# Kernel tuning notes

Hardware: AMD Instinct MI355X
Metric: run time of the kernel (lower is better)

## Reference

```python
import jax, jax.numpy as jnp
import numpy as np

EPS = 1e-7  # torchvision distance_box_iou_loss eps


def cxcywh_to_xyxy(b):
    cx, cy, w, h = b[..., 0], b[..., 1], b[..., 2], b[..., 3]
    return jnp.stack([cx - w / 2, cy - h / 2, cx + w / 2, cy + h / 2], axis=-1)


def iou_and_diou(b1, b2):
    # b1, b2: broadcastable [..., 4] in xyxy. Returns (plain iou, diou loss).
    x1, y1, x2, y2 = b1[..., 0], b1[..., 1], b1[..., 2], b1[..., 3]
    xg1, yg1, xg2, yg2 = b2[..., 0], b2[..., 1], b2[..., 2], b2[..., 3]
    xi1 = jnp.maximum(x1, xg1); yi1 = jnp.maximum(y1, yg1)
    xi2 = jnp.minimum(x2, xg2); yi2 = jnp.minimum(y2, yg2)
    inter = jnp.clip(xi2 - xi1, 0.0) * jnp.clip(yi2 - yi1, 0.0)
    union = (x2 - x1) * (y2 - y1) + (xg2 - xg1) * (yg2 - yg1) - inter
    iou = inter / union                 # ops.box_iou: no eps
    iou_e = inter / (union + EPS)       # distance_box_iou_loss: eps
    xc1 = jnp.minimum(x1, xg1); yc1 = jnp.minimum(y1, yg1)
    xc2 = jnp.maximum(x2, xg2); yc2 = jnp.maximum(y2, yg2)
    diag = (xc2 - xc1) ** 2 + (yc2 - yc1) ** 2 + EPS
    dist = ((x1 + x2 - xg1 - xg2) * 0.5) ** 2 + ((y1 + y2 - yg1 - yg2) * 0.5) ** 2
    return iou, 1.0 - iou_e + dist / diag


def bce(p, t):
    # torch binary_cross_entropy clamps log terms at -100
    lnp = jnp.maximum(jnp.log(p), -100.0)
    ln1 = jnp.maximum(jnp.log(1.0 - p), -100.0)
    return -(t * lnp + (1.0 - t) * ln1)


def hungarian(cost):
    # O(n^3) Hungarian (Kuhn-Munkres with potentials) on a square matrix.
    # Returns col assignment per row (row_ind = arange(n)). Matches scipy
    # linear_sum_assignment for square inputs.
    n = cost.shape[0]
    INF = np.inf
    u = np.zeros(n + 1); v = np.zeros(n + 1)
    p = np.zeros(n + 1, dtype=np.int64)
    way = np.zeros(n + 1, dtype=np.int64)
    for i in range(1, n + 1):
        p[0] = i
        j0 = 0
        minv = np.full(n + 1, INF)
        used = np.zeros(n + 1, dtype=bool)
        while True:
            used[j0] = True
            i0 = p[j0]
            cur = cost[i0 - 1] - u[i0] - v[1:]
            free = ~used[1:]
            upd = free & (cur < minv[1:])
            minv[1:] = np.where(upd, cur, minv[1:])
            way[1:] = np.where(upd, j0, way[1:])
            masked = np.where(free, minv[1:], INF)
            j1 = int(np.argmin(masked)) + 1
            delta = masked[j1 - 1]
            uidx = np.nonzero(used)[0]
            u[p[uidx]] += delta
            v[uidx] -= delta
            minv[1:] = np.where(free, minv[1:] - delta, minv[1:])
            j0 = j1
            if p[j0] == 0:
                break
        while j0:
            j1 = way[j0]
            p[j0] = p[j1]
            j0 = j1
    col_of_row = np.empty(n, dtype=np.int64)
    col_of_row[p[1:] - 1] = np.arange(n)
    return col_of_row


def build_cost_and_match(p, bbox_pred, labels_target, bbox_target):
    # Fused, fully vectorized replacement of the original O(N*M) python loop.
    pb = cxcywh_to_xyxy(bbox_pred)   # [B,N,4]
    tb = cxcywh_to_xyxy(bbox_target)  # [B,M,4]
    _, diou_pair = iou_and_diou(pb[:, :, None, :], tb[:, None, :, :])  # [B,N,M]
    # original uses reduction='mean' BCE/L1 over the batch -> batch-constant [N,M]
    label_cost = bce(p[:, :, None], labels_target[:, None, :]).mean(axis=0)  # [N,M]
    l1_cost = jnp.abs(bbox_pred[:, :, None, :] - bbox_target[:, None, :, :]).mean(axis=(0, 3))
    cost = diou_pair + label_cost[None] + l1_cost[None]  # [B,N,M]
    cost_np = np.asarray(jax.device_get(cost), dtype=np.float64)
    cols = np.stack([hungarian(cost_np[b]) for b in range(cost_np.shape[0])])
    return jnp.asarray(cols)  # [B,N]


def matched_losses(labels_pred, bbox_pred, labels_target, bbox_target, cols):
    p = jax.nn.sigmoid(labels_pred[..., 0])  # [B,N]
    B = p.shape[0]
    bi = jnp.arange(B)[:, None]
    # square matching: row indices are arange(N), only targets get permuted
    t_m = labels_target[bi, cols]   # [B,N]
    bt_m = bbox_target[bi, cols]    # [B,N,4]
    w = jax.lax.stop_gradient((t_m == 1.0).astype(p.dtype))  # positives mask
    iou_e, diou_e = iou_and_diou(cxcywh_to_xyxy(bbox_pred), cxcywh_to_xyxy(bt_m))
    wsum = w.sum()
    diou_loss = (diou_e * w).sum() / wsum
    iou = (iou_e * w).sum() / wsum
    label_loss = bce(p, t_m).mean()
    bbox_loss = (jnp.abs(bbox_pred - bt_m) * w[..., None]).sum() / (wsum * 4.0)
    return diou_loss + label_loss + bbox_loss, iou


def setup_inputs() -> dict:
    key = jax.random.key(0)
    k1, k2, k3, k4 = jax.random.split(key, 4)
    B, N, M = 64, 256, 256
    labels_pred = jax.random.normal(k1, (B, N, 1), dtype=jnp.float32)
    # cxcywh boxes in (0.05, 0.95) so areas/unions are strictly positive
    bbox_pred = jax.random.uniform(k2, (B, N, 4), dtype=jnp.float32) * 0.9 + 0.05
    labels_target = jax.random.randint(k3, (B, M), 0, 2).astype(jnp.float32)
    bbox_target = jax.random.uniform(k4, (B, M, 4), dtype=jnp.float32) * 0.9 + 0.05
    return {"labels_pred": labels_pred, "bbox_pred": bbox_pred,
            "labels_target": labels_target, "bbox_target": bbox_target}


def reference(labels_pred, bbox_pred, labels_target, bbox_target):
    p = jax.nn.sigmoid(labels_pred[..., 0])
    cols = build_cost_and_match(p, bbox_pred, labels_target, bbox_target)
    total_loss, iou = matched_losses(labels_pred, bbox_pred, labels_target, bbox_target, cols)
    return total_loss, iou
```

## Files before the change

### kernel.cpp

```cpp
#include <hip/hip_runtime.h>
#include <math.h>

#define BB 64
#define NN 256
#define MM 256
#define EPSF 1e-7f
#define ROWS_LDS 156


__device__ __forceinline__ void iou_diou(const float4 pb, const float4 tb,
                                         float& iou, float& diou) {
    float x1 = pb.x - pb.z * 0.5f, y1 = pb.y - pb.w * 0.5f;
    float x2 = pb.x + pb.z * 0.5f, y2 = pb.y + pb.w * 0.5f;
    float xg1 = tb.x - tb.z * 0.5f, yg1 = tb.y - tb.w * 0.5f;
    float xg2 = tb.x + tb.z * 0.5f, yg2 = tb.y + tb.w * 0.5f;
    float xi1 = fmaxf(x1, xg1), yi1 = fmaxf(y1, yg1);
    float xi2 = fminf(x2, xg2), yi2 = fminf(y2, yg2);
    float inter = fmaxf(xi2 - xi1, 0.f) * fmaxf(yi2 - yi1, 0.f);
    float uni = (x2 - x1) * (y2 - y1) + (xg2 - xg1) * (yg2 - yg1) - inter;
    iou = inter / uni;
    float iou_e = inter / (uni + EPSF);
    float xc1 = fminf(x1, xg1), yc1 = fminf(y1, yg1);
    float xc2 = fmaxf(x2, xg2), yc2 = fmaxf(y2, yg2);
    float dx = xc2 - xc1, dy = yc2 - yc1;
    float diag = dx * dx + dy * dy + EPSF;
    float ex = (x1 + x2 - xg1 - xg2) * 0.5f;
    float ey = (y1 + y2 - yg1 - yg2) * 0.5f;
    float dist = ex * ex + ey * ey;
    diou = 1.f - iou_e + dist / diag;
}

__device__ __forceinline__ unsigned long long dkey(double d, int j) {
    unsigned long long b = (unsigned long long)__double_as_longlong(d);
    b ^= (b >> 63) ? 0xFFFFFFFFFFFFFFFFULL : 0x8000000000000000ULL;
    return (b & ~511ULL) | (unsigned long long)j;
}
__device__ __forceinline__ double unkey(unsigned long long k) {
    unsigned long long b = k & ~511ULL;
    b ^= (b & 0x8000000000000000ULL) ? 0x8000000000000000ULL : 0xFFFFFFFFFFFFFFFFULL;
    return __longlong_as_double((long long)b);
}

#define SEL4I(s, a0, a1, a2, a3) ((s) == 0 ? (a0) : (s) == 1 ? (a1) : (s) == 2 ? (a2) : (a3))
#define SEL4D(s, a0, a1, a2, a3) ((s) == 0 ? (a0) : (s) == 1 ? (a1) : (s) == 2 ? (a2) : (a3))

__device__ __forceinline__ double readlane_d(double v, int lane) {
    unsigned long long b = (unsigned long long)__double_as_longlong(v);
    int lo = __builtin_amdgcn_readlane((int)(unsigned int)b, lane);
    int hi = __builtin_amdgcn_readlane((int)(unsigned int)(b >> 32), lane);
    return __longlong_as_double((long long)(((unsigned long long)(unsigned int)hi << 32) |
                                            (unsigned long long)(unsigned int)lo));
}

#define RED_DPP_K(CTRL)                                                                     \
    do {                                                                                    \
        int lo_ = (int)(unsigned int)ka, hi_ = (int)(unsigned int)(ka >> 32);               \
        int nlo_ = __builtin_amdgcn_update_dpp(lo_, lo_, CTRL, 0xF, 0xF, false);            \
        int nhi_ = __builtin_amdgcn_update_dpp(hi_, hi_, CTRL, 0xF, 0xF, false);            \
        unsigned long long ok_ = ((unsigned long long)(unsigned int)nhi_ << 32) |           \
                                 (unsigned long long)(unsigned int)nlo_;                    \
        if (ok_ < ka) ka = ok_;                                                             \
    } while (0)

#define RED_ALL()                                                                           \
    do {                                                                                    \
        RED_DPP_K(0x111); RED_DPP_K(0x112); RED_DPP_K(0x114); RED_DPP_K(0x118);             \
        RED_DPP_K(0x142); RED_DPP_K(0x143);                                                 \
        unsigned int klo_ = (unsigned int)__builtin_amdgcn_readlane((int)(unsigned int)ka, 63); \
        unsigned int khi_ = (unsigned int)__builtin_amdgcn_readlane((int)(unsigned int)(ka >> 32), 63); \
        ka = ((unsigned long long)khi_ << 32) | klo_;                                       \
    } while (0)

#define RED_U32_STEP(CTRL)                                                                  \
    do {                                                                                    \
        unsigned int n_ = (unsigned int)__builtin_amdgcn_update_dpp((int)kb, (int)kb, CTRL, 0xF, 0xF, false); \
        if (n_ < kb) kb = n_;                                                               \
    } while (0)
#define RED_U32_ALL()                                                                       \
    do {                                                                                    \
        RED_U32_STEP(0x111); RED_U32_STEP(0x112); RED_U32_STEP(0x114); RED_U32_STEP(0x118); \
        RED_U32_STEP(0x142); RED_U32_STEP(0x143);                                           \
        kb = (unsigned int)__builtin_amdgcn_readlane((int)kb, 63);                          \
    } while (0)

__global__ __launch_bounds__(256) void k_prep(const float* __restrict__ lp,
                                              float* __restrict__ A,
                                              float* __restrict__ C) {
    int idx = blockIdx.x * 256 + threadIdx.x;
    float x = lp[idx];
    float p = 1.f / (1.f + expf(-x));
    A[idx] = -fmaxf(logf(p), -100.f);
    C[idx] = -fmaxf(logf(1.f - p), -100.f);
}

__global__ __launch_bounds__(256) void k_nm(const float* __restrict__ A,
                                            const float* __restrict__ C,
                                            const float* __restrict__ bp,
                                            const float* __restrict__ bt,
                                            const float* __restrict__ lt,
                                            float* __restrict__ lc,
                                            float* __restrict__ l1c) {
    int n = blockIdx.x, m = threadIdx.x;
    float sl = 0.f, s1 = 0.f;
    for (int b = 0; b < BB; ++b) {
        float a = A[b * NN + n];
        float c = C[b * NN + n];
        float t = lt[b * MM + m];
        sl += t * a + (1.f - t) * c;
        float4 P = *reinterpret_cast<const float4*>(bp + ((size_t)b * NN + n) * 4);
        float4 T = *reinterpret_cast<const float4*>(bt + ((size_t)b * MM + m) * 4);
        s1 += fabsf(P.x - T.x) + fabsf(P.y - T.y) + fabsf(P.z - T.z) + fabsf(P.w - T.w);
    }
    lc[n * MM + m]  = sl * (1.f / 64.f);
    l1c[n * MM + m] = s1 * (1.f / 256.f);
}

__global__ __launch_bounds__(256) void k_cost(const float* __restrict__ bp,
                                              const float* __restrict__ bt,
                                              const float* __restrict__ lc,
                                              const float* __restrict__ l1c,
                                              float* __restrict__ cost) {
    int bn = blockIdx.x;
    int b = bn >> 8, n = bn & 255;
    int m = threadIdx.x;
    float4 P = *reinterpret_cast<const float4*>(bp + ((size_t)bn) * 4);
    float4 T = *reinterpret_cast<const float4*>(bt + ((size_t)b * MM + m) * 4);
    float iou, diou;
    iou_diou(P, T, iou, diou);
    cost[((size_t)bn << 8) + m] = diou + lc[(n << 8) + m] + l1c[(n << 8) + m];
}

__global__ __launch_bounds__(64) void k_hungarian(const float* __restrict__ cost,
                                                  int* __restrict__ cols) {
    const int b = blockIdx.x;
    const int lane = threadIdx.x;
    const float* Cm = cost + (size_t)b * NN * MM;
    const unsigned long long MAXK = 0xFFFFFFFFFFFFFFFFULL;
    const double INFD = __builtin_inf();

    __shared__ float ldsC[ROWS_LDS * MM];
    __shared__ float ldsU[NN];
    __shared__ int jofrow[NN + 1];
    __shared__ int matches[NN + 1];
    for (int r = lane; r <= NN; r += 64) { jofrow[r] = 0x7fffffff; matches[r] = 0; }
    __syncthreads();

    double cm0 = INFD, cm1 = INFD, cm2 = INFD, cm3 = INFD;
    int rm0 = 0, rm1 = 0, rm2 = 0, rm3 = 0;
    for (int i = 0; i < NN; ++i) {
        float4 cr = *reinterpret_cast<const float4*>(Cm + (size_t)i * MM + 4 * lane);
        if (i < ROWS_LDS) *reinterpret_cast<float4*>(&ldsC[i * MM + 4 * lane]) = cr;
        float rl = fminf(fminf(cr.x, cr.y), fminf(cr.z, cr.w));
        unsigned int kb = __float_as_uint(rl);
        RED_U32_ALL();
        float u0i = __uint_as_float(kb);
        if (lane == 0) ldsU[i] = u0i;
        double du = (double)u0i;
        double h0 = (double)cr.x - du;
        double h1 = (double)cr.y - du;
        double h2 = (double)cr.z - du;
        double h3 = (double)cr.w - du;
        if (h0 < cm0) { cm0 = h0; rm0 = i; }
        if (h1 < cm1) { cm1 = h1; rm1 = i; }
        if (h2 < cm2) { cm2 = h2; rm2 = i; }
        if (h3 < cm3) { cm3 = h3; rm3 = i; }
    }
    atomicMin(&jofrow[rm0 + 1], 4 * lane + 1);
    atomicMin(&jofrow[rm1 + 1], 4 * lane + 2);
    atomicMin(&jofrow[rm2 + 1], 4 * lane + 3);
    atomicMin(&jofrow[rm3 + 1], 4 * lane + 4);
    atomicAdd(&matches[rm0 + 1], 1);
    atomicAdd(&matches[rm1 + 1], 1);
    atomicAdd(&matches[rm2 + 1], 1);
    atomicAdd(&matches[rm3 + 1], 1);
    __syncthreads();

    double vj0 = cm0, vj1 = cm1, vj2 = cm2, vj3 = cm3;
    int pj0_ = (jofrow[rm0 + 1] == 4 * lane + 1) ? rm0 + 1 : 0;
    int pj1_ = (jofrow[rm1 + 1] == 4 * lane + 2) ? rm1 + 1 : 0;
    int pj2_ = (jofrow[rm2 + 1] == 4 * lane + 3) ? rm2 + 1 : 0;
    int pj3_ = (jofrow[rm3 + 1] == 4 * lane + 4) ? rm3 + 1 : 0;
    double up0 = pj0_ ? (double)ldsU[pj0_ - 1] : 0.0;
    double up1 = pj1_ ? (double)ldsU[pj1_ - 1] : 0.0;
    double up2 = pj2_ ? (double)ldsU[pj2_ - 1] : 0.0;
    double up3 = pj3_ ? (double)ldsU[pj3_ - 1] : 0.0;
    int wy0 = 0, wy1 = 0, wy2 = 0, wy3 = 0;

    unsigned long long am0 = __ballot(jofrow[1 + lane]       != 0x7fffffff);
    unsigned long long am1 = __ballot(jofrow[1 + 64 + lane]  != 0x7fffffff);
    unsigned long long am2 = __ballot(jofrow[1 + 128 + lane] != 0x7fffffff);
    unsigned long long am3 = __ballot(jofrow[1 + 192 + lane] != 0x7fffffff);

    for (int i = 1; i <= NN; ++i) {
        if (matches[i] != 1) continue;
        int j1 = jofrow[i];
        int o = (j1 - 1) >> 2, s = (j1 - 1) & 3;
        float4 cr;
        if (i - 1 < ROWS_LDS)
            cr = *reinterpret_cast<const float4*>(&ldsC[(i - 1) * MM + 4 * lane]);
        else
            cr = *reinterpret_cast<const float4*>(Cm + (size_t)(i - 1) * MM + 4 * lane);
        double du = (double)ldsU[i - 1];
        double h0 = ((double)cr.x - du) - vj0;
        double h1 = ((double)cr.y - du) - vj1;
        double h2 = ((double)cr.z - du) - vj2;
        double h3 = ((double)cr.w - du) - vj3;
        if (lane == o) {
            if (s == 0) h0 = INFD; else if (s == 1) h1 = INFD;
            else if (s == 2) h2 = INFD; else h3 = INFD;
        }
        double hm = fmin(fmin(h0, h1), fmin(h2, h3));
        unsigned long long ka = (unsigned long long)__double_as_longlong(hm);
        RED_ALL();
        double m = __longlong_as_double((long long)ka);
        if (lane == o) {
            if (s == 0)      { vj0 -= m; up0 += m; }
            else if (s == 1) { vj1 -= m; up1 += m; }
            else if (s == 2) { vj2 -= m; up2 += m; }
            else             { vj3 -= m; up3 += m; }
        }
    }

    for (int i = 1; i <= NN; ++i) {
        unsigned long long amv = (i <= 64) ? am0 : (i <= 128) ? am1 : (i <= 192) ? am2 : am3;
        if ((amv >> ((i - 1) & 63)) & 1ULL) continue;
        float4 cr;
        if (i - 1 < ROWS_LDS)
            cr = *reinterpret_cast<const float4*>(&ldsC[(i - 1) * MM + 4 * lane]);
        else
            cr = *reinterpret_cast<const float4*>(Cm + (size_t)(i - 1) * MM + 4 * lane);
        double du = (double)ldsU[i - 1];
        double h0 = ((double)cr.x - du) - vj0;
        double h1 = ((double)cr.y - du) - vj1;
        double h2 = ((double)cr.z - du) - vj2;
        double h3 = ((double)cr.w - du) - vj3;
        unsigned long long k0 = dkey(h0, 4 * lane + 1);
        unsigned long long k1 = dkey(h1, 4 * lane + 2);
        unsigned long long k2 = dkey(h2, 4 * lane + 3);
        unsigned long long k3 = dkey(h3, 4 * lane + 4);
        unsigned long long ea = k1 < k0 ? k1 : k0;
        unsigned long long eb = k3 < k2 ? k3 : k2;
        unsigned long long ka = eb < ea ? eb : ea;
        RED_ALL();
        int j1 = (int)(ka & 511ULL);
        int o1 = (j1 - 1) >> 2, s1 = (j1 - 1) & 3;
        int pcur = __builtin_amdgcn_readlane(SEL4I(s1, pj0_, pj1_, pj2_, pj3_), o1);
        if (pcur == 0) {
            double u_i = du + unkey(ka);
            if (lane == o1) {
                if (s1 == 0)      { pj0_ = i; up0 = u_i; }
                else if (s1 == 1) { pj1_ = i; up1 = u_i; }
                else if (s1 == 2) { pj2_ = i; up2 = u_i; }
                else              { pj3_ = i; up3 = u_i; }
            }
            unsigned long long bit = 1ULL << ((i - 1) & 63);
            if (i <= 64) am0 |= bit; else if (i <= 128) am1 |= bit;
            else if (i <= 192) am2 |= bit; else am3 |= bit;
        }
    }

    for (int i = 1; i <= NN; ++i) {
        unsigned long long amv = (i <= 64) ? am0 : (i <= 128) ? am1 : (i <= 192) ? am2 : am3;
        if ((amv >> ((i - 1) & 63)) & 1ULL) continue;

        double u_i = (double)ldsU[i - 1];
        double mv0 = INFD, mv1 = INFD, mv2 = INFD, mv3 = INFD;
        int used4 = 0;
        int j0 = 0;
        int i0 = i;
        double ui0 = u_i;

        for (int it = 0; it <= NN; ++it) {
            double uv0 = ui0 + vj0, uv1 = ui0 + vj1, uv2 = ui0 + vj2, uv3 = ui0 + vj3;
            float4 cr;
            if (i0 - 1 < ROWS_LDS)
                cr = *reinterpret_cast<const float4*>(&ldsC[(i0 - 1) * MM + 4 * lane]);
            else
                cr = *reinterpret_cast<const float4*>(Cm + (size_t)(i0 - 1) * MM + 4 * lane);

            if (!(used4 & 1)) { double cur = (double)cr.x - uv0; if (cur < mv0) { mv0 = cur; wy0 = j0; } }
            if (!(used4 & 2)) { double cur = (double)cr.y - uv1; if (cur < mv1) { mv1 = cur; wy1 = j0; } }
            if (!(used4 & 4)) { double cur = (double)cr.z - uv2; if (cur < mv2) { mv2 = cur; wy2 = j0; } }
            if (!(used4 & 8)) { double cur = (double)cr.w - uv3; if (cur < mv3) { mv3 = cur; wy3 = j0; } }

            unsigned long long k0 = (used4 & 1) ? MAXK : dkey(mv0, 4 * lane + 1);
            unsigned long long k1 = (used4 & 2) ? MAXK : dkey(mv1, 4 * lane + 2);
            unsigned long long k2 = (used4 & 4) ? MAXK : dkey(mv2, 4 * lane + 3);
            unsigned long long k3 = (used4 & 8) ? MAXK : dkey(mv3, 4 * lane + 4);

            unsigned long long ea = k1 < k0 ? k1 : k0;
            unsigned long long eb = k3 < k2 ? k3 : k2;
            unsigned long long ka = eb < ea ? eb : ea;

            RED_ALL();

            double delta = unkey(ka);
            int j1 = (int)(ka & 511ULL);
            int o1 = (j1 - 1) >> 2, s1 = (j1 - 1) & 3;
            int pa = __builtin_amdgcn_readlane(SEL4I(s1, pj0_, pj1_, pj2_, pj3_), o1);
            double ua = readlane_d(SEL4D(s1, up0, up1, up2, up3), o1);

            u_i += delta;
            if (used4 & 1) { up0 += delta; vj0 -= delta; } else { mv0 -= delta; }
            if (used4 & 2) { up1 += delta; vj1 -= delta; } else { mv1 -= delta; }
            if (used4 & 4) { up2 += delta; vj2 -= delta; } else { mv2 -= delta; }
            if (used4 & 8) { up3 += delta; vj3 -= delta; } else { mv3 -= delta; }

            j0 = j1;
            if (pa == 0) break;
            int ci = j1 - 1;
            if ((ci >> 2) == lane) used4 |= 1 << (ci & 3);
            i0 = pa;
            ui0 = ua;
        }

        int jj = j0;
        while (jj) {
            int o = (jj - 1) >> 2, s = (jj - 1) & 3;
            int wv = SEL4I(s, wy0, wy1, wy2, wy3);
            int jn = __builtin_amdgcn_readlane(wv, o);
            int pn; double un;
            if (jn == 0) { pn = i; un = u_i; }
            else {
                int o2 = (jn - 1) >> 2, s2 = (jn - 1) & 3;
                int pv = SEL4I(s2, pj0_, pj1_, pj2_, pj3_);
                double uv = SEL4D(s2, up0, up1, up2, up3);
                pn = __builtin_amdgcn_readlane(pv, o2);
                un = readlane_d(uv, o2);
            }
            if (lane == o) {
                if (s == 0)      { pj0_ = pn; up0 = un; }
                else if (s == 1) { pj1_ = pn; up1 = un; }
                else if (s == 2) { pj2_ = pn; up2 = un; }
                else             { pj3_ = pn; up3 = un; }
            }
            jj = jn;
        }
    }

    cols[b * NN + (pj0_ - 1)] = 4 * lane + 0;
    cols[b * NN + (pj1_ - 1)] = 4 * lane + 1;
    cols[b * NN + (pj2_ - 1)] = 4 * lane + 2;
    cols[b * NN + (pj3_ - 1)] = 4 * lane + 3;
}

__global__ __launch_bounds__(256) void k_loss(const float* __restrict__ lp,
                                              const float* __restrict__ bp,
                                              const float* __restrict__ lt,
                                              const float* __restrict__ bt,
                                              const int* __restrict__ cols,
                                              float* __restrict__ partials) {
    int b = blockIdx.x, n = threadIdx.x;
    int col = cols[b * NN + n];
    float x = lp[b * NN + n];
    float pp = 1.f / (1.f + expf(-x));
    float t = lt[b * MM + col];
    float4 P = *reinterpret_cast<const float4*>(bp + ((size_t)b * NN + n) * 4);
    float4 T = *reinterpret_cast<const float4*>(bt + ((size_t)b * MM + col) * 4);
    float w = (t == 1.f) ? 1.f : 0.f;
    float iou, diou;
    iou_diou(P, T, iou, diou);
    float bce = -(t * fmaxf(logf(pp), -100.f) + (1.f - t) * fmaxf(logf(1.f - pp), -100.f));
    float l1 = fabsf(P.x - T.x) + fabsf(P.y - T.y) + fabsf(P.z - T.z) + fabsf(P.w - T.w);

    float v0 = w, v1 = diou * w, v2 = iou * w, v3 = bce, v4 = l1 * w;
    #pragma unroll
    for (int mm = 1; mm < 64; mm <<= 1) {
        v0 += __shfl_xor(v0, mm); v1 += __shfl_xor(v1, mm);
        v2 += __shfl_xor(v2, mm); v3 += __shfl_xor(v3, mm);
        v4 += __shfl_xor(v4, mm);
    }
    __shared__ float red[4][5];
    int wid = n >> 6, lane = n & 63;
    if (lane == 0) { red[wid][0] = v0; red[wid][1] = v1; red[wid][2] = v2; red[wid][3] = v3; red[wid][4] = v4; }
    __syncthreads();
    if (n == 0) {
        float s0 = red[0][0] + red[1][0] + red[2][0] + red[3][0];
        float s1 = red[0][1] + red[1][1] + red[2][1] + red[3][1];
        float s2 = red[0][2] + red[1][2] + red[2][2] + red[3][2];
        float s3 = red[0][3] + red[1][3] + red[2][3] + red[3][3];
        float s4 = red[0][4] + red[1][4] + red[2][4] + red[3][4];
        partials[b * 8 + 0] = s0; partials[b * 8 + 1] = s1; partials[b * 8 + 2] = s2;
        partials[b * 8 + 3] = s3; partials[b * 8 + 4] = s4;
    }
}

__global__ __launch_bounds__(64) void k_final(const float* __restrict__ partials,
                                              float* __restrict__ out) {
    int t = threadIdx.x;
    float v0 = partials[t * 8 + 0], v1 = partials[t * 8 + 1], v2 = partials[t * 8 + 2];
    float v3 = partials[t * 8 + 3], v4 = partials[t * 8 + 4];
    #pragma unroll
    for (int mm = 1; mm < 64; mm <<= 1) {
        v0 += __shfl_xor(v0, mm); v1 += __shfl_xor(v1, mm);
        v2 += __shfl_xor(v2, mm); v3 += __shfl_xor(v3, mm);
        v4 += __shfl_xor(v4, mm);
    }
    if (t == 0) {
        float wsum = v0;
        float diou_loss = v1 / wsum;
        float iou = v2 / wsum;
        float label_loss = v3 * (1.f / (64.f * 256.f));
        float bbox_loss = v4 / (wsum * 4.f);
        out[0] = diou_loss + label_loss + bbox_loss;
        out[1] = iou;
    }
}

extern "C" void kernel_launch(void* const* d_in, const int* in_sizes, int n_in,
                              void* d_out, int out_size, void* d_ws, size_t ws_size,
                              hipStream_t stream) {
    const float* labels_pred   = (const float*)d_in[0];
    const float* bbox_pred     = (const float*)d_in[1];
    const float* labels_target = (const float*)d_in[2];
    const float* bbox_target   = (const float*)d_in[3];
    float* out = (float*)d_out;

    float* A    = (float*)d_ws;
    float* C    = A + BB * NN;
    float* lc   = C + BB * NN;
    float* l1c  = lc + NN * MM;
    float* cost = l1c + NN * MM;
    int*   cols = (int*)(cost + (size_t)BB * NN * MM);
    float* partials = (float*)(cols + BB * NN);

    k_prep<<<BB * NN / 256, 256, 0, stream>>>(labels_pred, A, C);
    k_nm<<<NN, MM, 0, stream>>>(A, C, bbox_pred, bbox_target, labels_target, lc, l1c);
    k_cost<<<BB * NN, MM, 0, stream>>>(bbox_pred, bbox_target, lc, l1c, cost);
    k_hungarian<<<BB, 64, 0, stream>>>(cost, cols);
    k_loss<<<BB, NN, 0, stream>>>(labels_pred, bbox_pred, labels_target, bbox_target, cols, partials);
    k_final<<<1, 64, 0, stream>>>(partials, out);
}
```

Baseline: 2.454 ms.

## Speculatively prefetch next Hungarian row during cross-row reduction

In the Hungarian augmenting loop, the per-lane argmin reduction now carries the matched row index along with the key. After the intra-row DPP steps, it reads the four 16-lane group winners and loads all four candidate cost rows before the final cross-row reduction finishes. The correct row is then selected by group, which takes the next row load off the serial critical path. The price is four row loads per iteration instead of one, an extra DPP per step, and higher register pressure.

```diff
diff --git a/kernel.cpp b/kernel.cpp
--- a/kernel.cpp
+++ b/kernel.cpp
@@ -62,6 +62,17 @@
         if (ok_ < ka) ka = ok_;                                                             \
     } while (0)
 
+#define RED_DPP_P(CTRL)                                                                     \
+    do {                                                                                    \
+        int lo_ = (int)(unsigned int)ka, hi_ = (int)(unsigned int)(ka >> 32);               \
+        int nlo_ = __builtin_amdgcn_update_dpp(lo_, lo_, CTRL, 0xF, 0xF, false);            \
+        int nhi_ = __builtin_amdgcn_update_dpp(hi_, hi_, CTRL, 0xF, 0xF, false);            \
+        int npa_ = __builtin_amdgcn_update_dpp(pa_l, pa_l, CTRL, 0xF, 0xF, false);          \
+        unsigned long long ok_ = ((unsigned long long)(unsigned int)nhi_ << 32) |           \
+                                 (unsigned long long)(unsigned int)nlo_;                    \
+        if (ok_ < ka) { ka = ok_; pa_l = npa_; }                                            \
+    } while (0)
+
 #define RED_ALL()                                                                           \
     do {                                                                                    \
         RED_DPP_K(0x111); RED_DPP_K(0x112); RED_DPP_K(0x114); RED_DPP_K(0x118);             \
@@ -144,6 +155,10 @@
     __shared__ int matches[NN + 1];
     for (int r = lane; r <= NN; r += 64) { jofrow[r] = 0x7fffffff; matches[r] = 0; }
     __syncthreads();
+
+    #define LOAD_ROW(r) ((r) - 1 < ROWS_LDS                                                  \
+        ? *reinterpret_cast<const float4*>(&ldsC[((r) - 1) * MM + 4 * lane])                 \
+        : *reinterpret_cast<const float4*>(Cm + (size_t)((r) - 1) * MM + 4 * lane))
 
     double cm0 = INFD, cm1 = INFD, cm2 = INFD, cm3 = INFD;
     int rm0 = 0, rm1 = 0, rm2 = 0, rm3 = 0;
@@ -195,11 +210,7 @@
         if (matches[i] != 1) continue;
         int j1 = jofrow[i];
         int o = (j1 - 1) >> 2, s = (j1 - 1) & 3;
-        float4 cr;
-        if (i - 1 < ROWS_LDS)
-            cr = *reinterpret_cast<const float4*>(&ldsC[(i - 1) * MM + 4 * lane]);
-        else
-            cr = *reinterpret_cast<const float4*>(Cm + (size_t)(i - 1) * MM + 4 * lane);
+        float4 cr = LOAD_ROW(i);
         double du = (double)ldsU[i - 1];
         double h0 = ((double)cr.x - du) - vj0;
         double h1 = ((double)cr.y - du) - vj1;
@@ -224,11 +235,7 @@
     for (int i = 1; i <= NN; ++i) {
         unsigned long long amv = (i <= 64) ? am0 : (i <= 128) ? am1 : (i <= 192) ? am2 : am3;
         if ((amv >> ((i - 1) & 63)) & 1ULL) continue;
-        float4 cr;
-        if (i - 1 < ROWS_LDS)
-            cr = *reinterpret_cast<const float4*>(&ldsC[(i - 1) * MM + 4 * lane]);
-        else
-            cr = *reinterpret_cast<const float4*>(Cm + (size_t)(i - 1) * MM + 4 * lane);
+        float4 cr = LOAD_ROW(i);
         double du = (double)ldsU[i - 1];
         double h0 = ((double)cr.x - du) - vj0;
         double h1 = ((double)cr.y - du) - vj1;
@@ -267,16 +274,11 @@
         double mv0 = INFD, mv1 = INFD, mv2 = INFD, mv3 = INFD;
         int used4 = 0;
         int j0 = 0;
-        int i0 = i;
         double ui0 = u_i;
+        float4 cr = LOAD_ROW(i);
 
         for (int it = 0; it <= NN; ++it) {
             double uv0 = ui0 + vj0, uv1 = ui0 + vj1, uv2 = ui0 + vj2, uv3 = ui0 + vj3;
-            float4 cr;
-            if (i0 - 1 < ROWS_LDS)
-                cr = *reinterpret_cast<const float4*>(&ldsC[(i0 - 1) * MM + 4 * lane]);
-            else
-                cr = *reinterpret_cast<const float4*>(Cm + (size_t)(i0 - 1) * MM + 4 * lane);
 
             if (!(used4 & 1)) { double cur = (double)cr.x - uv0; if (cur < mv0) { mv0 = cur; wy0 = j0; } }
             if (!(used4 & 2)) { double cur = (double)cr.y - uv1; if (cur < mv1) { mv1 = cur; wy1 = j0; } }
@@ -288,16 +290,35 @@
             unsigned long long k2 = (used4 & 4) ? MAXK : dkey(mv2, 4 * lane + 3);
             unsigned long long k3 = (used4 & 8) ? MAXK : dkey(mv3, 4 * lane + 4);
 
-            unsigned long long ea = k1 < k0 ? k1 : k0;
-            unsigned long long eb = k3 < k2 ? k3 : k2;
-            unsigned long long ka = eb < ea ? eb : ea;
-
-            RED_ALL();
+            unsigned long long ka; int pa_l;
+            if (k1 < k0) { ka = k1; pa_l = pj1_; } else { ka = k0; pa_l = pj0_; }
+            unsigned long long kb2; int pb2;
+            if (k3 < k2) { kb2 = k3; pb2 = pj3_; } else { kb2 = k2; pb2 = pj2_; }
+            if (kb2 < ka) { ka = kb2; pa_l = pb2; }
+
+            RED_DPP_P(0x111); RED_DPP_P(0x112); RED_DPP_P(0x114); RED_DPP_P(0x118);
+
+            int pc0 = __builtin_amdgcn_readlane(pa_l, 15);
+            int pc1 = __builtin_amdgcn_readlane(pa_l, 31);
+            int pc2 = __builtin_amdgcn_readlane(pa_l, 47);
+            int pc3 = __builtin_amdgcn_readlane(pa_l, 63);
+            float4 cc0 = LOAD_ROW(pc0 > 0 ? pc0 : 1);
+            float4 cc1 = LOAD_ROW(pc1 > 0 ? pc1 : 1);
+            float4 cc2 = LOAD_ROW(pc2 > 0 ? pc2 : 1);
+            float4 cc3 = LOAD_ROW(pc3 > 0 ? pc3 : 1);
+
+            RED_DPP_K(0x142); RED_DPP_K(0x143);
+            {
+                unsigned int klo = (unsigned int)__builtin_amdgcn_readlane((int)(unsigned int)ka, 63);
+                unsigned int khi = (unsigned int)__builtin_amdgcn_readlane((int)(unsigned int)(ka >> 32), 63);
+                ka = ((unsigned long long)khi << 32) | klo;
+            }
 
             double delta = unkey(ka);
             int j1 = (int)(ka & 511ULL);
             int o1 = (j1 - 1) >> 2, s1 = (j1 - 1) & 3;
-            int pa = __builtin_amdgcn_readlane(SEL4I(s1, pj0_, pj1_, pj2_, pj3_), o1);
+            int g = o1 >> 4;
+            int pa = (g == 0) ? pc0 : (g == 1) ? pc1 : (g == 2) ? pc2 : pc3;
             double ua = readlane_d(SEL4D(s1, up0, up1, up2, up3), o1);
 
             u_i += delta;
@@ -310,8 +331,8 @@
             if (pa == 0) break;
             int ci = j1 - 1;
             if ((ci >> 2) == lane) used4 |= 1 << (ci & 3);
-            i0 = pa;
             ui0 = ua;
+            cr = (g == 0) ? cc0 : (g == 1) ? cc1 : (g == 2) ? cc2 : cc3;
         }
 
         int jj = j0;
@@ -342,6 +363,7 @@
     cols[b * NN + (pj1_ - 1)] = 4 * lane + 1;
     cols[b * NN + (pj2_ - 1)] = 4 * lane + 2;
     cols[b * NN + (pj3_ - 1)] = 4 * lane + 3;
+    #undef LOAD_ROW
 }
 
 __global__ __launch_bounds__(256) void k_loss(const float* __restrict__ lp,
```

Result: slower. 2.721 ms (+10.9%).
